# Kernel tuning notes

Hardware: AMD Instinct MI355X
Metric: run time of the kernel (lower is better)

The kernel has to match this reference:

```python
import jax, jax.numpy as jnp
import numpy as np

N = 38332          # poi_len - 1 nodes
POI_LEN = 38333
GF = 64            # graph_features
POI_DIM = 128
C = 128            # gcn_channel
L = 4              # gcn_layers
OUT = 128          # graph_out_dim
E = N * 16         # edges (avg degree 16)
IN_DIM = POI_DIM * GF // 2 + GF // 2  # 4128


def leaky(x, s):
    return jnp.where(x >= 0, x, s * x)


def _gcn(x, W, b, src, dst):
    # PyG GCNConv: lin -> symmetric deg^{-1/2} norm over self-loop graph -> scatter-sum + bias
    h = x @ W
    deg = jax.ops.segment_sum(jnp.ones(src.shape[0], h.dtype), dst, num_segments=N)
    dinv = jnp.where(deg > 0, jax.lax.rsqrt(deg), 0.0)
    norm = dinv[src] * dinv[dst]
    return jax.ops.segment_sum(h[src] * norm[:, None], dst, num_segments=N) + b


def _gat(x, W, a_src, a_dst, b, src, dst):
    # PyG GATConv (heads=1): per-edge LeakyReLU(0.2) logits, softmax over incoming edges
    h = x @ W
    als = h @ a_src            # [N]
    ald = h @ a_dst            # [N]
    e = leaky(als[src] + ald[dst], 0.2)   # [E+N]
    m = jax.ops.segment_max(e, dst, num_segments=N)
    ex = jnp.exp(e - m[dst])
    s = jax.ops.segment_sum(ex, dst, num_segments=N)
    alpha = ex / s[dst]
    return jax.ops.segment_sum(h[src] * alpha[:, None], dst, num_segments=N) + b


def _gnorm(x, w, b, ms, eps=1e-5):
    # PyG GraphNorm over the single graph (node axis)
    mean = x.mean(axis=0)
    out = x - ms * mean
    var = (out * out).mean(axis=0)
    return w * out * jax.lax.rsqrt(var + eps) + b


def setup_inputs() -> dict:
    key = jax.random.key(0)
    ks = jax.random.split(key, 20)
    d = {}
    d["poi"] = jax.random.randint(ks[0], (N, GF // 2), 0, POI_LEN, dtype=jnp.int32)
    d["distance"] = jax.random.uniform(ks[1], (N, GF // 2), dtype=jnp.float32)
    d["edge_index"] = jax.random.randint(ks[2], (2, E), 0, N, dtype=jnp.int32)
    d["emb_table"] = jax.random.normal(ks[3], (POI_LEN, POI_DIM), dtype=jnp.float32) * 0.05
    d["W_in"] = jax.random.normal(ks[4], (IN_DIM, C), dtype=jnp.float32) * 0.02
    d["b_in"] = jnp.zeros((C,), jnp.float32)
    d["gcn_W"] = jax.random.normal(ks[5], (L, C, C), dtype=jnp.float32) * 0.05
    d["gcn_b"] = jnp.zeros((L, C), jnp.float32)
    d["norm_w"] = jnp.ones((L, C), jnp.float32)
    d["norm_b"] = jnp.zeros((L, C), jnp.float32)
    d["norm_ms"] = jnp.ones((L, C), jnp.float32)
    d["gat_W"] = jax.random.normal(ks[6], (L, C, C), dtype=jnp.float32) * 0.05
    d["gat_asrc"] = jax.random.normal(ks[7], (L, C), dtype=jnp.float32) * 0.05
    d["gat_adst"] = jax.random.normal(ks[8], (L, C), dtype=jnp.float32) * 0.05
    d["gat_b"] = jnp.zeros((L, C), jnp.float32)
    d["W_out"] = jax.random.normal(ks[9], (C, 1), dtype=jnp.float32) * 0.05
    d["b_out"] = jnp.zeros((1,), jnp.float32)
    d["fc1_W"] = jax.random.normal(ks[10], (N, 128), dtype=jnp.float32) * 0.01
    d["fc1_b"] = jnp.zeros((128,), jnp.float32)
    d["fc2_W"] = jax.random.normal(ks[11], (128, OUT), dtype=jnp.float32) * 0.05
    d["fc2_b"] = jnp.zeros((OUT,), jnp.float32)
    return d


def reference(poi, distance, edge_index, emb_table, W_in, b_in, gcn_W, gcn_b,
              norm_w, norm_b, norm_ms, gat_W, gat_asrc, gat_adst, gat_b,
              W_out, b_out, fc1_W, fc1_b, fc2_W, fc2_b):
    loops = jnp.arange(N, dtype=edge_index.dtype)
    src = jnp.concatenate([edge_index[0], loops])   # self loops (PyG default)
    dst = jnp.concatenate([edge_index[1], loops])
    # feature assembly: emb(poi) flattened || distance
    x = jnp.concatenate([emb_table[poi].reshape(N, -1), distance], axis=1)  # [N, 4128]
    x = leaky(_gcn(x, W_in, b_in, src, dst), 0.01)
    for i in range(L):  # GcnUnit: GCN->norm->lrelu->res, GAT->norm->lrelu->res (shared norm params)
        t = _gnorm(_gcn(x, gcn_W[i], gcn_b[i], src, dst), norm_w[i], norm_b[i], norm_ms[i])
        x = x + leaky(t, 0.01)
        t = _gnorm(_gat(x, gat_W[i], gat_asrc[i], gat_adst[i], gat_b[i], src, dst),
                   norm_w[i], norm_b[i], norm_ms[i])
        x = x + leaky(t, 0.01)
    x = leaky(_gcn(x, W_out, b_out, src, dst), 0.01).reshape(-1)  # [N]
    h = leaky(x @ fc1_W + fc1_b, 0.01)
    return h @ fc2_W + fc2_b  # [128]
```

## Files before the change

kernel.cpp:

```cpp
#include <hip/hip_runtime.h>


typedef _Float16 f16;
typedef f16 f16x8 __attribute__((ext_vector_type(8)));
typedef f16 f16x4 __attribute__((ext_vector_type(4)));
typedef f16 f16x2 __attribute__((ext_vector_type(2)));
typedef float f32x4 __attribute__((ext_vector_type(4)));

__device__ __forceinline__ float lrelu(float x, float s){ return x>=0.f? x : s*x; }

__global__ __launch_bounds__(256) void k_deg(const int* __restrict__ dst,
                                             int* __restrict__ deg, int E) {
  int i = blockIdx.x * 256 + threadIdx.x;
  if (i < E) atomicAdd(&deg[dst[i]], 1);
}

__global__ __launch_bounds__(1024) void k_scan1(const int* __restrict__ deg,
    int* __restrict__ row_ptr, int* __restrict__ bsum, float* __restrict__ dinv, int n) {
  int b = blockIdx.x, t = threadIdx.x, i = b * 1024 + t;
  __shared__ int sd[1024];
  int v = (i < n) ? deg[i] : 0;
  if (i < n) dinv[i] = rsqrtf((float)(v + 1));
  sd[t] = v;
  __syncthreads();
  for (int off = 1; off < 1024; off <<= 1) {
    int o = (t >= off) ? sd[t - off] : 0;
    __syncthreads();
    sd[t] += o;
    __syncthreads();
  }
  if (i < n) row_ptr[i + 1] = sd[t];
  if (t == 1023) bsum[b] = sd[1023];
  if (b == 0 && t == 0) row_ptr[0] = 0;
}

__global__ __launch_bounds__(64) void k_scan2(int* __restrict__ bsum, int nb) {
  int lane = threadIdx.x;
  int v = (lane < nb) ? bsum[lane] : 0;
  int x = v;
  for (int off = 1; off < 64; off <<= 1) {
    int o = __shfl_up(x, off, 64);
    if (lane >= off) x += o;
  }
  if (lane < nb) bsum[lane] = x - v;
}

__global__ __launch_bounds__(256) void k_scan3(int* __restrict__ row_ptr,
                                               const int* __restrict__ bsum, int n) {
  int i = blockIdx.x * 256 + threadIdx.x;
  if (i < n) row_ptr[i + 1] += bsum[i >> 10];
}

__global__ __launch_bounds__(256) void k_fill(const int* __restrict__ src,
                                              const int* __restrict__ dst,
                                              const int* __restrict__ row_ptr,
                                              const float* __restrict__ dinv,
                                              int* __restrict__ fill,
                                              int* __restrict__ csr,
                                              float* __restrict__ csrw, int E) {
  int i = blockIdx.x * 256 + threadIdx.x;
  if (i < E) {
    int d = dst[i], s = src[i];
    int pos = row_ptr[d] + atomicAdd(&fill[d], 1);
    csr[pos] = s;
    csrw[pos] = dinv[d] * dinv[s];
  }
}

__global__ __launch_bounds__(256) void k_conv_emb(const float* __restrict__ src,
                                                  f16* __restrict__ dst, int total4) {
  int i = blockIdx.x * 256 + threadIdx.x;
  if (i >= total4) return;
  float4 v = ((const float4*)src)[i];
  f16x4 o = { (f16)v.x, (f16)v.y, (f16)v.z, (f16)v.w };
  ((f16x4*)dst)[i] = o;
}

__global__ __launch_bounds__(256) void k_pack_w(const float* __restrict__ W,
    f16* __restrict__ hi, int kb_total) {
  int idx = blockIdx.x * 256 + threadIdx.x;
  int c = idx & 127, kb = idx >> 7;
  if (kb >= kb_total) return;
  f16x8 hv;
#pragma unroll
  for (int j = 0; j < 8; j++) hv[j] = (f16)W[(size_t)(kb*8 + j) * 128 + c];
  ((f16x8*)hi)[idx] = hv;
}

__global__ __launch_bounds__(256) void k_pack_w8(const float* __restrict__ gcnW,
    const float* __restrict__ gatW, f16* __restrict__ hi, f16* __restrict__ lo) {
  int mat = blockIdx.y;
  const float* W = (mat < 4) ? gcnW + (size_t)mat * 16384 : gatW + (size_t)(mat - 4) * 16384;
  int idx = blockIdx.x * 256 + threadIdx.x;
  int c = idx & 127, kb = idx >> 7;
  f16x8 hv, lv;
#pragma unroll
  for (int j = 0; j < 8; j++) {
    float v = W[(size_t)(kb*8 + j) * 128 + c];
    f16 h = (f16)v;
    hv[j] = h; lv[j] = (f16)(v - (float)h);
  }
  ((f16x8*)hi)[mat * 2048 + idx] = hv;
  ((f16x8*)lo)[mat * 2048 + idx] = lv;
}

#define APAD 152
__global__ __launch_bounds__(512) void k_mfma_embed(const int* __restrict__ poi,
    const float* __restrict__ dist, const f16* __restrict__ eh,
    const f16* __restrict__ wh, f16* __restrict__ H16, int n) {
  __shared__ __attribute__((aligned(16))) char smem[49152];
  int* poi_s = (int*)smem;
  f16* aS    = (f16*)(smem + 8192);
  f16* OT    = (f16*)smem;
  float* F   = (float*)(smem + 16384);
  int tid = threadIdx.x;
  int bn = blockIdx.x * 64;
  int half = tid >> 8;
  int t2 = tid & 255;
  int ln = t2 >> 2, qt = t2 & 3;
  int xrow = bn + ln; if (xrow > n - 1) xrow = n - 1;
  {
#pragma unroll
    for (int jj = 0; jj < 4; jj++)
      poi_s[half * 1024 + (qt * 4 + jj) * 64 + ln] =
        poi[(size_t)xrow * 32 + half * 16 + qt * 4 + jj];
  }
  int w2 = (tid >> 6) & 3, lane = tid & 63;
  int q = lane >> 4, l15 = lane & 15;
  int mtb = (w2 & 1) * 2;
  int ntb = (w2 >> 1) * 4;
  f16* aH = aS + half * 64 * APAD;
  f32x4 acc[2][4];
#pragma unroll
  for (int a = 0; a < 2; a++)
#pragma unroll
    for (int b = 0; b < 4; b++) { acc[a][b][0]=0.f; acc[a][b][1]=0.f; acc[a][b][2]=0.f; acc[a][b][3]=0.f; }
  __syncthreads();

  f16x8 r0, r1, r2, r3;
  {
    const f16* srcp = eh + (size_t)poi_s[half * 1024 + ln] * 128 + qt * 32;
    r0 = *(const f16x8*)(srcp);      r1 = *(const f16x8*)(srcp + 8);
    r2 = *(const f16x8*)(srcp + 16); r3 = *(const f16x8*)(srcp + 24);
  }

#pragma unroll 1
  for (int j = 0; j < 16; j++) {
    __syncthreads();
    f16* wp = aH + ln * APAD + qt * 32;
    *(f16x8*)(wp) = r0; *(f16x8*)(wp + 8) = r1;
    *(f16x8*)(wp + 16) = r2; *(f16x8*)(wp + 24) = r3;
    if (j + 1 < 16) {
      const f16* srcp = eh + (size_t)poi_s[half * 1024 + (j + 1) * 64 + ln] * 128 + qt * 32;
      r0 = *(const f16x8*)(srcp);      r1 = *(const f16x8*)(srcp + 8);
      r2 = *(const f16x8*)(srcp + 16); r3 = *(const f16x8*)(srcp + 24);
    }
    __syncthreads();
#pragma unroll
    for (int kcl = 0; kcl < 4; kcl++) {
      f16x8 a_h[2];
#pragma unroll
      for (int mi = 0; mi < 2; mi++)
        a_h[mi] = *(const f16x8*)(aH + ((mtb + mi) * 16 + l15) * APAD + kcl * 32 + q * 8);
      int kb = (half * 16 + j) * 16 + kcl * 4 + q;
#pragma unroll
      for (int ni = 0; ni < 4; ni++) {
        f16x8 bh = *(const f16x8*)(wh + ((size_t)kb * 128 + (ntb + ni) * 16 + l15) * 8);
#pragma unroll
        for (int mi = 0; mi < 2; mi++)
          acc[mi][ni] = __builtin_amdgcn_mfma_f32_16x16x32_f16(a_h[mi], bh, acc[mi][ni], 0, 0, 0);
      }
    }
  }
  if (half) {
    int nc0 = bn + (mtb + 0) * 16 + l15; if (nc0 > n - 1) nc0 = n - 1;
    int nc1 = bn + (mtb + 1) * 16 + l15; if (nc1 > n - 1) nc1 = n - 1;
    f16x8 ad[2];
#pragma unroll
    for (int mi = 0; mi < 2; mi++) {
      int nc = mi ? nc1 : nc0;
      const float* dp = dist + (size_t)nc * 32 + q * 8;
      float4 d0 = *(const float4*)dp, d1 = *(const float4*)(dp + 4);
      ad[mi][0]=(f16)d0.x; ad[mi][1]=(f16)d0.y; ad[mi][2]=(f16)d0.z; ad[mi][3]=(f16)d0.w;
      ad[mi][4]=(f16)d1.x; ad[mi][5]=(f16)d1.y; ad[mi][6]=(f16)d1.z; ad[mi][7]=(f16)d1.w;
    }
    int kb = 512 + q;
#pragma unroll
    for (int ni = 0; ni < 4; ni++) {
      f16x8 bh = *(const f16x8*)(wh + ((size_t)kb * 128 + (ntb + ni) * 16 + l15) * 8);
#pragma unroll
      for (int mi = 0; mi < 2; mi++)
        acc[mi][ni] = __builtin_amdgcn_mfma_f32_16x16x32_f16(ad[mi], bh, acc[mi][ni], 0, 0, 0);
    }
  }
  __syncthreads();
  if (half) {
#pragma unroll
    for (int mi = 0; mi < 2; mi++)
#pragma unroll
      for (int ni = 0; ni < 4; ni++)
#pragma unroll
        for (int r = 0; r < 4; r++)
          F[((mtb + mi) * 16 + q * 4 + r) * 128 + (ntb + ni) * 16 + l15] = acc[mi][ni][r];
  }
  __syncthreads();
  if (!half) {
#pragma unroll
    for (int mi = 0; mi < 2; mi++)
#pragma unroll
      for (int ni = 0; ni < 4; ni++)
#pragma unroll
        for (int r = 0; r < 4; r++) {
          int o = ((mtb + mi) * 16 + q * 4 + r) * 128 + (ntb + ni) * 16 + l15;
          OT[o] = (f16)(acc[mi][ni][r] + F[o]);
        }
  }
  __syncthreads();
#pragma unroll
  for (int ch = 0; ch < 2; ch++) {
    int c1024 = tid + ch * 512;
    int row = c1024 >> 4, c8 = c1024 & 15;
    if (bn + row < n)
      *(f16x8*)(H16 + (size_t)(bn + row) * 128 + c8 * 8) = *(const f16x8*)(OT + row * 128 + c8 * 8);
  }
}

#define LPAD 136
__global__ __launch_bounds__(256) void k_mfma_lin(const f16* __restrict__ XH,
    const f16* __restrict__ wh, const f16* __restrict__ wl,
    f16* __restrict__ H16, int n,
    const float* __restrict__ asrc, const float* __restrict__ adst,
    float* __restrict__ als, float* __restrict__ ald) {
  __shared__ __attribute__((aligned(16))) char smem[64 * LPAD * 2];
  f16* aS = (f16*)smem;
  f16* ot = (f16*)smem;
  float* dsrc = (float*)(smem + 16384);
  float* ddst = (float*)(smem + 16896);
  int tid = threadIdx.x;
  int bn = blockIdx.x * 64;
  int ln = tid >> 2, qt = tid & 3;
  int xrow = bn + ln; if (xrow > n - 1) xrow = n - 1;
  int w = tid >> 6, lane = tid & 63;
  int q = lane >> 4, l15 = lane & 15;
  int mtb = (w & 1) * 2;
  int ntb = (w >> 1) * 4;
  {
    const f16* srcp = XH + (size_t)xrow * 128 + qt * 32;
    f16* wp = aS + ln * LPAD + qt * 32;
    *(f16x8*)(wp)      = *(const f16x8*)(srcp);
    *(f16x8*)(wp + 8)  = *(const f16x8*)(srcp + 8);
    *(f16x8*)(wp + 16) = *(const f16x8*)(srcp + 16);
    *(f16x8*)(wp + 24) = *(const f16x8*)(srcp + 24);
  }
  float av[4], bv[4];
  if (asrc) {
#pragma unroll
    for (int ni = 0; ni < 4; ni++) {
      av[ni] = asrc[(ntb + ni) * 16 + l15];
      bv[ni] = adst[(ntb + ni) * 16 + l15];
    }
  }
  f32x4 acc[2][4];
#pragma unroll
  for (int a = 0; a < 2; a++)
#pragma unroll
    for (int b = 0; b < 4; b++) { acc[a][b][0]=0.f; acc[a][b][1]=0.f; acc[a][b][2]=0.f; acc[a][b][3]=0.f; }
  __syncthreads();
#pragma unroll
  for (int kcl = 0; kcl < 4; kcl++) {
    f16x8 a_h[2];
#pragma unroll
    for (int mi = 0; mi < 2; mi++)
      a_h[mi] = *(const f16x8*)(aS + ((mtb + mi) * 16 + l15) * LPAD + kcl * 32 + q * 8);
    int kb = kcl * 4 + q;
#pragma unroll
    for (int ni = 0; ni < 4; ni++) {
      size_t boff = ((size_t)kb * 128 + (ntb + ni) * 16 + l15) * 8;
      f16x8 bh = *(const f16x8*)(wh + boff);
      f16x8 bl = *(const f16x8*)(wl + boff);
#pragma unroll
      for (int mi = 0; mi < 2; mi++) {
        acc[mi][ni] = __builtin_amdgcn_mfma_f32_16x16x32_f16(a_h[mi], bh, acc[mi][ni], 0, 0, 0);
        acc[mi][ni] = __builtin_amdgcn_mfma_f32_16x16x32_f16(a_h[mi], bl, acc[mi][ni], 0, 0, 0);
      }
    }
  }
  __syncthreads();
  if (asrc) {
#pragma unroll
    for (int mi = 0; mi < 2; mi++)
#pragma unroll
      for (int r = 0; r < 4; r++) {
        float ps = 0.f, pd = 0.f;
#pragma unroll
        for (int ni = 0; ni < 4; ni++) { ps += acc[mi][ni][r] * av[ni]; pd += acc[mi][ni][r] * bv[ni]; }
#pragma unroll
        for (int msk = 8; msk > 0; msk >>= 1) {
          ps += __shfl_xor(ps, msk, 64);
          pd += __shfl_xor(pd, msk, 64);
        }
        if (l15 == 0) {
          int row = (mtb + mi) * 16 + q * 4 + r;
          dsrc[row * 2 + (w >> 1)] = ps;
          ddst[row * 2 + (w >> 1)] = pd;
        }
      }
  }
#pragma unroll
  for (int mi = 0; mi < 2; mi++)
#pragma unroll
    for (int ni = 0; ni < 4; ni++)
#pragma unroll
      for (int r = 0; r < 4; r++)
        ot[((mtb + mi) * 16 + q * 4 + r) * 128 + (ntb + ni) * 16 + l15] = (f16)acc[mi][ni][r];
  __syncthreads();
  if (bn + ln < n) {
    f16* dst = H16 + (size_t)(bn + ln) * 128 + qt * 32;
    const f16* srcp = ot + ln * 128 + qt * 32;
#pragma unroll
    for (int jj = 0; jj < 4; jj++)
      *(f16x8*)(dst + jj * 8) = *(const f16x8*)(srcp + jj * 8);
  }
  if (asrc && tid < 64 && bn + tid < n) {
    als[bn + tid] = dsrc[tid * 2] + dsrc[tid * 2 + 1];
    ald[bn + tid] = ddst[tid * 2] + ddst[tid * 2 + 1];
  }
}

__global__ __launch_bounds__(256) void k_gcn_agg16(const f16x2* __restrict__ H2,
    const float* __restrict__ dinv, const int* __restrict__ row_ptr,
    const int* __restrict__ csr, const float* __restrict__ csrw,
    const float* __restrict__ bias,
    float2* __restrict__ out2, f16x2* __restrict__ xh_out, int n, int leaky_flag,
    float* __restrict__ psum, float* __restrict__ psumsq) {
  int w = threadIdx.x >> 6;
  int node = blockIdx.x * 4 + w;
  int lane = threadIdx.x & 63;
  __shared__ float s1[4][128], s2[4][128];
  float vx = 0.f, vy = 0.f;
  if (node < n) {
    int rs = row_ptr[node], re = row_ptr[node + 1];
    int d = re - rs;
    float dn = dinv[node];
    int  sidx = (lane < d) ? csr[rs + lane]  : 0;
    float swt = (lane < d) ? csrw[rs + lane] : 0.f;
    f16x2 sv = H2[(size_t)node * 64 + lane];
    float ax = dn * dn * (float)sv[0], ay = dn * dn * (float)sv[1];
    int dl = d < 64 ? d : 64;
    int j = 0;
#pragma unroll 4
    for (; j + 3 < dl; j += 4) {
      int i0 = __shfl(sidx, j, 64), i1 = __shfl(sidx, j + 1, 64);
      int i2 = __shfl(sidx, j + 2, 64), i3 = __shfl(sidx, j + 3, 64);
      float w0 = __shfl(swt, j, 64), w1 = __shfl(swt, j + 1, 64);
      float w2 = __shfl(swt, j + 2, 64), w3 = __shfl(swt, j + 3, 64);
      f16x2 v0 = H2[(size_t)i0 * 64 + lane];
      f16x2 v1 = H2[(size_t)i1 * 64 + lane];
      f16x2 v2 = H2[(size_t)i2 * 64 + lane];
      f16x2 v3 = H2[(size_t)i3 * 64 + lane];
      ax += w0*(float)v0[0] + w1*(float)v1[0] + w2*(float)v2[0] + w3*(float)v3[0];
      ay += w0*(float)v0[1] + w1*(float)v1[1] + w2*(float)v2[1] + w3*(float)v3[1];
    }
    for (; j < dl; j++) {
      int ii = __shfl(sidx, j, 64);
      float ww = __shfl(swt, j, 64);
      f16x2 v = H2[(size_t)ii * 64 + lane];
      ax += ww * (float)v[0]; ay += ww * (float)v[1];
    }
    for (int e = rs + 64; e < re; e++) {
      int s = csr[e]; float wv = csrw[e];
      f16x2 v = H2[(size_t)s * 64 + lane];
      ax += wv * (float)v[0]; ay += wv * (float)v[1];
    }
    float2 bvv = ((const float2*)bias)[lane];
    vx = ax + bvv.x; vy = ay + bvv.y;
    if (leaky_flag) { vx = lrelu(vx, 0.01f); vy = lrelu(vy, 0.01f); }
    out2[(size_t)node * 64 + lane] = make_float2(vx, vy);
    if (xh_out) { f16x2 o = { (f16)vx, (f16)vy }; xh_out[(size_t)node * 64 + lane] = o; }
  }
  if (psum) {
    s1[w][2*lane] = vx;  s1[w][2*lane+1] = vy;
    s2[w][2*lane] = vx*vx; s2[w][2*lane+1] = vy*vy;
    __syncthreads();
    int t = threadIdx.x;
    if (t < 128) {
      float S = s1[0][t] + s1[1][t] + s1[2][t] + s1[3][t];
      float Q = s2[0][t] + s2[1][t] + s2[2][t] + s2[3][t];
      int slot = blockIdx.x & 127;
      atomicAdd(&psum[slot * 128 + t], S);
      atomicAdd(&psumsq[slot * 128 + t], Q);
    }
  }
}

__global__ __launch_bounds__(256) void k_gat_agg16(const f16x2* __restrict__ H2,
    const float* __restrict__ als, const float* __restrict__ ald,
    const int* __restrict__ row_ptr, const int* __restrict__ csr,
    const float* __restrict__ bias, float2* __restrict__ y2, int n,
    float* __restrict__ psum, float* __restrict__ psumsq) {
  int w = threadIdx.x >> 6;
  int node = blockIdx.x * 4 + w;
  int lane = threadIdx.x & 63;
  __shared__ float s1[4][128], s2[4][128];
  float vx = 0.f, vy = 0.f;
  if (node < n) {
    int rs = row_ptr[node], re = row_ptr[node + 1];
    int d = re - rs;
    float aldn = ald[node];
    float e_self = lrelu(als[node] + aldn, 0.2f);
    f16x2 sv = H2[(size_t)node * 64 + lane];
    float ax, ay, sm;
    if (d <= 64) {
      int sidx = (lane < d) ? csr[rs + lane] : 0;
      float e_k = (lane < d) ? lrelu(als[sidx] + aldn, 0.2f) : -3.4e38f;
      float tmx = e_k;
      for (int off = 1; off < 64; off <<= 1) tmx = fmaxf(tmx, __shfl_xor(tmx, off, 64));
      float mx = fmaxf(e_self, tmx);
      float g_k = (lane < d) ? __expf(e_k - mx) : 0.f;
      float tsm = g_k;
      for (int off = 1; off < 64; off <<= 1) tsm += __shfl_xor(tsm, off, 64);
      float ws = __expf(e_self - mx);
      sm = tsm + ws;
      ax = ws * (float)sv[0]; ay = ws * (float)sv[1];
      int j = 0;
#pragma unroll 4
      for (; j + 3 < d; j += 4) {
        int i0 = __shfl(sidx, j, 64), i1 = __shfl(sidx, j + 1, 64);
        int i2 = __shfl(sidx, j + 2, 64), i3 = __shfl(sidx, j + 3, 64);
        float g0 = __shfl(g_k, j, 64), g1 = __shfl(g_k, j + 1, 64);
        float g2 = __shfl(g_k, j + 2, 64), g3 = __shfl(g_k, j + 3, 64);
        f16x2 v0 = H2[(size_t)i0 * 64 + lane];
        f16x2 v1 = H2[(size_t)i1 * 64 + lane];
        f16x2 v2 = H2[(size_t)i2 * 64 + lane];
        f16x2 v3 = H2[(size_t)i3 * 64 + lane];
        ax += g0*(float)v0[0] + g1*(float)v1[0] + g2*(float)v2[0] + g3*(float)v3[0];
        ay += g0*(float)v0[1] + g1*(float)v1[1] + g2*(float)v2[1] + g3*(float)v3[1];
      }
      for (; j < d; j++) {
        int ii = __shfl(sidx, j, 64);
        float gg = __shfl(g_k, j, 64);
        f16x2 v = H2[(size_t)ii * 64 + lane];
        ax += gg * (float)v[0]; ay += gg * (float)v[1];
      }
    } else {
      float mx = e_self;
      for (int i = rs + lane; i < re; i += 64) mx = fmaxf(mx, lrelu(als[csr[i]] + aldn, 0.2f));
      for (int off = 1; off < 64; off <<= 1) mx = fmaxf(mx, __shfl_xor(mx, off, 64));
      float ws = __expf(e_self - mx);
      sm = ws;
      ax = ws * (float)sv[0]; ay = ws * (float)sv[1];
      for (int i = rs; i < re; i++) {
        int s = csr[i];
        float g = __expf(lrelu(als[s] + aldn, 0.2f) - mx);
        f16x2 v = H2[(size_t)s * 64 + lane];
        sm += g; ax += g*(float)v[0]; ay += g*(float)v[1];
      }
    }
    float inv_s = 1.f / sm;
    float2 bvv = ((const float2*)bias)[lane];
    vx = ax * inv_s + bvv.x; vy = ay * inv_s + bvv.y;
    y2[(size_t)node * 64 + lane] = make_float2(vx, vy);
  }
  s1[w][2*lane] = vx;  s1[w][2*lane+1] = vy;
  s2[w][2*lane] = vx*vx; s2[w][2*lane+1] = vy*vy;
  __syncthreads();
  int t = threadIdx.x;
  if (t < 128) {
    float S = s1[0][t] + s1[1][t] + s1[2][t] + s1[3][t];
    float Q = s2[0][t] + s2[1][t] + s2[2][t] + s2[3][t];
    int slot = blockIdx.x & 127;
    atomicAdd(&psum[slot * 128 + t], S);
    atomicAdd(&psumsq[slot * 128 + t], Q);
  }
}

__global__ __launch_bounds__(256) void k_stats(const float* __restrict__ psum,
    const float* __restrict__ psumsq, const float* __restrict__ w,
    const float* __restrict__ bb, const float* __restrict__ ms,
    float* __restrict__ scaleA, float* __restrict__ shiftA, int n) {
  int t = threadIdx.x, c = t & 127, half = t >> 7;
  float S = 0.f, Q = 0.f;
  for (int s = half; s < 128; s += 2) { S += psum[s * 128 + c]; Q += psumsq[s * 128 + c]; }
  __shared__ float sh[256], sq[256];
  sh[t] = S; sq[t] = Q;
  __syncthreads();
  if (half == 0) {
    double Sd = (double)sh[c] + (double)sh[c + 128];
    double Qd = (double)sq[c] + (double)sq[c + 128];
    double invn = 1.0 / (double)n;
    double mean = Sd * invn;
    double mt = (double)ms[c] * mean;
    double var = Qd * invn - 2.0 * mt * mean + mt * mt;
    float rstd = rsqrtf((float)var + 1e-5f);
    float sc = w[c] * rstd;
    scaleA[c] = sc;
    shiftA[c] = bb[c] - sc * (float)mt;
  }
}

__global__ __launch_bounds__(256) void k_residual(const float* __restrict__ y,
    const float* __restrict__ scaleA, const float* __restrict__ shiftA,
    float* __restrict__ x, f16x4* __restrict__ xh, int n4) {
  int i = blockIdx.x * 256 + threadIdx.x;
  if (i >= n4) return;
  int c4 = (i & 31) * 4;
  float4 yv = ((const float4*)y)[i];
  float4 xv = ((float4*)x)[i];
  float4 sc = *(const float4*)(scaleA + c4);
  float4 sh = *(const float4*)(shiftA + c4);
  xv.x += lrelu(sc.x * yv.x + sh.x, 0.01f);
  xv.y += lrelu(sc.y * yv.y + sh.y, 0.01f);
  xv.z += lrelu(sc.z * yv.z + sh.z, 0.01f);
  xv.w += lrelu(sc.w * yv.w + sh.w, 0.01f);
  ((float4*)x)[i] = xv;
  if (xh) { f16x4 o = { (f16)xv.x, (f16)xv.y, (f16)xv.z, (f16)xv.w }; xh[i] = o; }
}

__global__ __launch_bounds__(256) void k_dot1(const float* __restrict__ x,
                                              const float* __restrict__ wv,
                                              float* __restrict__ o, int n) {
  int node = blockIdx.x * 4 + (threadIdx.x >> 6);
  int lane = threadIdx.x & 63;
  if (node >= n) return;
  float2 hv = ((const float2*)x)[(size_t)node * 64 + lane];
  float2 v1 = ((const float2*)wv)[lane];
  float s1 = hv.x * v1.x + hv.y * v1.y;
  for (int off = 32; off > 0; off >>= 1) s1 += __shfl_down(s1, off, 64);
  if (lane == 0) o[node] = s1;
}

__global__ __launch_bounds__(256) void k_scalar_agg(const float* __restrict__ xsv,
    const float* __restrict__ dinv, const int* __restrict__ row_ptr,
    const int* __restrict__ csr, const float* __restrict__ csrw,
    const float* __restrict__ b_out, float* __restrict__ xout, int n) {
  int i = blockIdx.x * 256 + threadIdx.x;
  if (i >= n) return;
  float dn = dinv[i];
  float acc = dn * dn * xsv[i];
  int re = row_ptr[i + 1];
  for (int e = row_ptr[i]; e < re; e++)
    acc += csrw[e] * xsv[csr[e]];
  xout[i] = lrelu(acc + b_out[0], 0.01f);
}

__global__ __launch_bounds__(256) void k_fc1(const float* __restrict__ xout,
    const float* __restrict__ fw, float* __restrict__ pfc, int n, int chunk) {
  int b = blockIdx.x, t = threadIdx.x;
  int c = t & 127, half = t >> 7;
  int s0 = b * chunk;
  int s1 = s0 + chunk; if (s1 > n) s1 = n;
  float s = 0.f;
  for (int i = s0 + half; i < s1; i += 2) s += xout[i] * fw[(size_t)i * 128 + c];
  __shared__ float sh[256];
  sh[t] = s; __syncthreads();
  if (half == 0) pfc[b * 128 + c] = sh[c] + sh[c + 128];
}

__global__ __launch_bounds__(128) void k_final(const float* __restrict__ pfc,
    const float* __restrict__ b1, const float* __restrict__ fw2,
    const float* __restrict__ b2, float* __restrict__ out) {
  int c = threadIdx.x;
  float s = 0.f;
  for (int b = 0; b < 128; b++) s += pfc[b * 128 + c];
  float hv = lrelu(s + b1[c], 0.01f);
  __shared__ float h1[128];
  h1[c] = hv; __syncthreads();
  float o = b2[c];
  for (int j = 0; j < 128; j++) o += h1[j] * fw2[j * 128 + c];
  out[c] = o;
}

extern "C" void kernel_launch(void* const* d_in, const int* in_sizes, int n_in,
                              void* d_out, int out_size, void* d_ws, size_t ws_size,
                              hipStream_t stream) {
  const int* poi      = (const int*)d_in[0];
  const float* dist   = (const float*)d_in[1];
  const int* ei       = (const int*)d_in[2];
  const float* emb    = (const float*)d_in[3];
  const float* W_in   = (const float*)d_in[4];
  const float* b_in   = (const float*)d_in[5];
  const float* gcn_W  = (const float*)d_in[6];
  const float* gcn_b  = (const float*)d_in[7];
  const float* norm_w = (const float*)d_in[8];
  const float* norm_b = (const float*)d_in[9];
  const float* norm_ms= (const float*)d_in[10];
  const float* gat_W  = (const float*)d_in[11];
  const float* gat_as = (const float*)d_in[12];
  const float* gat_ad = (const float*)d_in[13];
  const float* gat_b  = (const float*)d_in[14];
  const float* W_out  = (const float*)d_in[15];
  const float* b_out  = (const float*)d_in[16];
  const float* fc1_W  = (const float*)d_in[17];
  const float* fc1_b  = (const float*)d_in[18];
  const float* fc2_W  = (const float*)d_in[19];
  const float* fc2_b  = (const float*)d_in[20];

  const int N   = in_sizes[0] / 32;
  const int E   = in_sizes[2] / 2;
  const int POI = in_sizes[3] / 128;
  const int* srcp = ei;
  const int* dstp = ei + E;
  float* out = (float*)d_out;

  char* p = (char*)d_ws;
  auto alloc = [&](size_t bytes) { char* r = p; p += (bytes + 255) & ~(size_t)255; return r; };
  float* x   = (float*)alloc((size_t)N * 128 * 4);
  f16* h16   = (f16*)alloc((size_t)N * 128 * 2);
  f16* xh    = (f16*)alloc((size_t)N * 128 * 2);
  size_t Rneed = (size_t)POI * 128 * 2;
  size_t Ry    = (size_t)N * 128 * 4;
  char* R = alloc(Rneed > Ry ? Rneed : Ry);
  f16* ehalf = (f16*)R;
  float* y   = (float*)R;
  const int KBIN = 4128 / 8;
  f16* wih = (f16*)alloc((size_t)KBIN * 128 * 8 * 2);
  f16* wsh = (f16*)alloc((size_t)8 * 16384 * 2);
  f16* wsl = (f16*)alloc((size_t)8 * 16384 * 2);
  float* dinv   = (float*)alloc((size_t)N * 4);
  float* als    = (float*)alloc((size_t)N * 4);
  float* ald    = (float*)alloc((size_t)N * 4);
  float* xsv    = (float*)alloc((size_t)N * 4);
  float* xout   = (float*)alloc((size_t)N * 4);
  float* statsbuf = (float*)alloc((size_t)32 * 16384 * 4);
  float* pfc    = (float*)alloc(128 * 128 * 4);
  float* scaleA = (float*)alloc(128 * 4);
  float* shiftA = (float*)alloc(128 * 4);
  int* deg     = (int*)alloc((size_t)N * 2 * 4);
  int* fill    = deg + N;
  int* row_ptr = (int*)alloc(((size_t)N + 1) * 4);
  int* csr     = (int*)alloc((size_t)E * 4);
  float* csrw  = (float*)alloc((size_t)E * 4);
  int* bsum    = (int*)alloc(64 * 4);

  const int chunk = (N + 127) / 128;
  const int gblocks = (N + 63) / 64;
  const int eblocks = (E + 255) / 256;
  const int n4 = N * 32;
  const int nwb = (N + 3) / 4;
  const int nb1024 = (N + 1023) / 1024;

  hipMemsetAsync(deg, 0, sizeof(int) * 2 * (size_t)N, stream);
  hipMemsetAsync(statsbuf, 0, (size_t)32 * 16384 * 4, stream);
  k_deg<<<eblocks, 256, 0, stream>>>(dstp, deg, E);
  k_scan1<<<nb1024, 1024, 0, stream>>>(deg, row_ptr, bsum, dinv, N);
  k_scan2<<<1, 64, 0, stream>>>(bsum, nb1024);
  k_scan3<<<(N + 255) / 256, 256, 0, stream>>>(row_ptr, bsum, N);
  k_fill<<<eblocks, 256, 0, stream>>>(srcp, dstp, row_ptr, dinv, fill, csr, csrw, E);

  int et4 = POI * 128 / 4;
  k_conv_emb<<<(et4 + 255) / 256, 256, 0, stream>>>(emb, ehalf, et4);
  k_pack_w<<<(KBIN * 128 + 255) / 256, 256, 0, stream>>>(W_in, wih, KBIN);
  k_pack_w8<<<dim3(8, 8), 256, 0, stream>>>(gcn_W, gat_W, wsh, wsl);

  k_mfma_embed<<<gblocks, 512, 0, stream>>>(poi, dist, ehalf, wih, h16, N);
  k_gcn_agg16<<<nwb, 256, 0, stream>>>((const f16x2*)h16, dinv, row_ptr, csr, csrw, b_in,
                                       (float2*)x, (f16x2*)xh, N, 1, nullptr, nullptr);

  for (int l = 0; l < 4; l++) {
    const f16* gh = wsh + (size_t)l * 16384;
    const f16* gl = wsl + (size_t)l * 16384;
    const f16* th = wsh + (size_t)(4 + l) * 16384;
    const f16* tl = wsl + (size_t)(4 + l) * 16384;
    float* ps0 = statsbuf + (size_t)(4 * l) * 16384;
    float* pq0 = ps0 + 16384;
    float* ps1 = ps0 + 2 * 16384;
    float* pq1 = ps0 + 3 * 16384;
    k_mfma_lin<<<gblocks, 256, 0, stream>>>(xh, gh, gl, h16, N,
                                            (const float*)nullptr, (const float*)nullptr,
                                            (float*)nullptr, (float*)nullptr);
    k_gcn_agg16<<<nwb, 256, 0, stream>>>((const f16x2*)h16, dinv, row_ptr, csr, csrw,
                                         gcn_b + l * 128, (float2*)y, (f16x2*)nullptr, N, 0,
                                         ps0, pq0);
    k_stats<<<1, 256, 0, stream>>>(ps0, pq0, norm_w + l * 128, norm_b + l * 128,
                                   norm_ms + l * 128, scaleA, shiftA, N);
    k_residual<<<(n4 + 255) / 256, 256, 0, stream>>>(y, scaleA, shiftA, x, (f16x4*)xh, n4);
    k_mfma_lin<<<gblocks, 256, 0, stream>>>(xh, th, tl, h16, N,
                                            gat_as + l * 128, gat_ad + l * 128, als, ald);
    k_gat_agg16<<<nwb, 256, 0, stream>>>((const f16x2*)h16, als, ald, row_ptr, csr,
                                         gat_b + l * 128, (float2*)y, N, ps1, pq1);
    k_stats<<<1, 256, 0, stream>>>(ps1, pq1, norm_w + l * 128, norm_b + l * 128,
                                   norm_ms + l * 128, scaleA, shiftA, N);
    k_residual<<<(n4 + 255) / 256, 256, 0, stream>>>(y, scaleA, shiftA, x,
        (l == 3) ? (f16x4*)nullptr : (f16x4*)xh, n4);
  }

  k_dot1<<<nwb, 256, 0, stream>>>(x, W_out, xsv, N);
  k_scalar_agg<<<(N + 255) / 256, 256, 0, stream>>>(xsv, dinv, row_ptr, csr, csrw, b_out, xout, N);
  k_fc1<<<128, 256, 0, stream>>>(xout, fc1_W, pfc, N, chunk);
  k_final<<<1, 128, 0, stream>>>(pfc, fc1_b, fc2_W, fc2_b, out);
}
```

Measured before the change: 1.010 ms.

## Fuse residual/norm into linear loads, store aggregates as f16, widen gather

Removes the separate residual kernel: the GraphNorm scale/shift, leaky ReLU and residual add are now applied while the MFMA linear kernel loads its input tile, and for the last layer inside the final dot kernel. Aggregation outputs are stored as half precision instead of float32, and the f16 copy of x is dropped. The gather loops now have each half-wave process alternate edges with 4-wide f16 loads, combining the halves through a cross-lane shuffle. This cuts launches and intermediate memory traffic, at the cost of extra rounding from storing the normalized input in half precision.

Result: no change. 1.019 ms (+0.9%).

```diff
diff --git a/kernel.cpp b/kernel.cpp
--- a/kernel.cpp
+++ b/kernel.cpp
@@ -226,7 +226,9 @@
 }
 
 #define LPAD 136
-__global__ __launch_bounds__(256) void k_mfma_lin(const f16* __restrict__ XH,
+__global__ __launch_bounds__(256) void k_mfma_lin(float* __restrict__ X,
+    const f16* __restrict__ Y, const float* __restrict__ scaleA,
+    const float* __restrict__ shiftA,
     const f16* __restrict__ wh, const f16* __restrict__ wl,
     f16* __restrict__ H16, int n,
     const float* __restrict__ asrc, const float* __restrict__ adst,
@@ -239,18 +241,38 @@
   int tid = threadIdx.x;
   int bn = blockIdx.x * 64;
   int ln = tid >> 2, qt = tid & 3;
-  int xrow = bn + ln; if (xrow > n - 1) xrow = n - 1;
+  int xrow = bn + ln; bool valid = xrow < n; if (!valid) xrow = n - 1;
   int w = tid >> 6, lane = tid & 63;
   int q = lane >> 4, l15 = lane & 15;
   int mtb = (w & 1) * 2;
   int ntb = (w >> 1) * 4;
   {
-    const f16* srcp = XH + (size_t)xrow * 128 + qt * 32;
+    float* xp = X + (size_t)xrow * 128 + qt * 32;
     f16* wp = aS + ln * LPAD + qt * 32;
-    *(f16x8*)(wp)      = *(const f16x8*)(srcp);
-    *(f16x8*)(wp + 8)  = *(const f16x8*)(srcp + 8);
-    *(f16x8*)(wp + 16) = *(const f16x8*)(srcp + 16);
-    *(f16x8*)(wp + 24) = *(const f16x8*)(srcp + 24);
+    if (Y) {
+      const f16* yp = Y + (size_t)xrow * 128 + qt * 32;
+#pragma unroll
+      for (int cc = 0; cc < 32; cc += 4) {
+        float4 xv = *(const float4*)(xp + cc);
+        f16x4 yv = *(const f16x4*)(yp + cc);
+        float4 sc = *(const float4*)(scaleA + qt * 32 + cc);
+        float4 sh = *(const float4*)(shiftA + qt * 32 + cc);
+        xv.x += lrelu(sc.x * (float)yv[0] + sh.x, 0.01f);
+        xv.y += lrelu(sc.y * (float)yv[1] + sh.y, 0.01f);
+        xv.z += lrelu(sc.z * (float)yv[2] + sh.z, 0.01f);
+        xv.w += lrelu(sc.w * (float)yv[3] + sh.w, 0.01f);
+        if (valid) *(float4*)(xp + cc) = xv;
+        f16x4 st = { (f16)xv.x, (f16)xv.y, (f16)xv.z, (f16)xv.w };
+        *(f16x4*)(wp + cc) = st;
+      }
+    } else {
+#pragma unroll
+      for (int cc = 0; cc < 32; cc += 4) {
+        float4 xv = *(const float4*)(xp + cc);
+        f16x4 st = { (f16)xv.x, (f16)xv.y, (f16)xv.z, (f16)xv.w };
+        *(f16x4*)(wp + cc) = st;
+      }
+    }
   }
   float av[4], bv[4];
   if (asrc) {
@@ -327,60 +349,78 @@
   }
 }
 
-__global__ __launch_bounds__(256) void k_gcn_agg16(const f16x2* __restrict__ H2,
+__global__ __launch_bounds__(256) void k_gcn_agg16(const f16x4* __restrict__ H4,
     const float* __restrict__ dinv, const int* __restrict__ row_ptr,
     const int* __restrict__ csr, const float* __restrict__ csrw,
     const float* __restrict__ bias,
-    float2* __restrict__ out2, f16x2* __restrict__ xh_out, int n, int leaky_flag,
+    float4* __restrict__ xout4, f16x4* __restrict__ y4, int n, int leaky_flag,
     float* __restrict__ psum, float* __restrict__ psumsq) {
   int w = threadIdx.x >> 6;
   int node = blockIdx.x * 4 + w;
   int lane = threadIdx.x & 63;
+  int half = lane >> 5, li = lane & 31;
   __shared__ float s1[4][128], s2[4][128];
-  float vx = 0.f, vy = 0.f;
+  float o0=0.f,o1=0.f,o2=0.f,o3=0.f;
   if (node < n) {
     int rs = row_ptr[node], re = row_ptr[node + 1];
     int d = re - rs;
     float dn = dinv[node];
     int  sidx = (lane < d) ? csr[rs + lane]  : 0;
     float swt = (lane < d) ? csrw[rs + lane] : 0.f;
-    f16x2 sv = H2[(size_t)node * 64 + lane];
-    float ax = dn * dn * (float)sv[0], ay = dn * dn * (float)sv[1];
+    float a0, a1, a2, a3;
+    {
+      f16x4 v = H4[(size_t)node * 32 + li];
+      float wv = 0.5f * dn * dn;
+      a0 = wv*(float)v[0]; a1 = wv*(float)v[1]; a2 = wv*(float)v[2]; a3 = wv*(float)v[3];
+    }
     int dl = d < 64 ? d : 64;
     int j = 0;
-#pragma unroll 4
-    for (; j + 3 < dl; j += 4) {
-      int i0 = __shfl(sidx, j, 64), i1 = __shfl(sidx, j + 1, 64);
-      int i2 = __shfl(sidx, j + 2, 64), i3 = __shfl(sidx, j + 3, 64);
-      float w0 = __shfl(swt, j, 64), w1 = __shfl(swt, j + 1, 64);
-      float w2 = __shfl(swt, j + 2, 64), w3 = __shfl(swt, j + 3, 64);
-      f16x2 v0 = H2[(size_t)i0 * 64 + lane];
-      f16x2 v1 = H2[(size_t)i1 * 64 + lane];
-      f16x2 v2 = H2[(size_t)i2 * 64 + lane];
-      f16x2 v3 = H2[(size_t)i3 * 64 + lane];
-      ax += w0*(float)v0[0] + w1*(float)v1[0] + w2*(float)v2[0] + w3*(float)v3[0];
-      ay += w0*(float)v0[1] + w1*(float)v1[1] + w2*(float)v2[1] + w3*(float)v3[1];
-    }
-    for (; j < dl; j++) {
+    for (; j + 7 < dl; j += 8) {
+      int i0 = __shfl(sidx, j + half, 64),     i1 = __shfl(sidx, j + 2 + half, 64);
+      int i2 = __shfl(sidx, j + 4 + half, 64), i3 = __shfl(sidx, j + 6 + half, 64);
+      float w0 = __shfl(swt, j + half, 64),     w1 = __shfl(swt, j + 2 + half, 64);
+      float w2 = __shfl(swt, j + 4 + half, 64), w3 = __shfl(swt, j + 6 + half, 64);
+      f16x4 v0 = H4[(size_t)i0 * 32 + li];
+      f16x4 v1 = H4[(size_t)i1 * 32 + li];
+      f16x4 v2 = H4[(size_t)i2 * 32 + li];
+      f16x4 v3 = H4[(size_t)i3 * 32 + li];
+      a0 += w0*(float)v0[0] + w1*(float)v1[0] + w2*(float)v2[0] + w3*(float)v3[0];
+      a1 += w0*(float)v0[1] + w1*(float)v1[1] + w2*(float)v2[1] + w3*(float)v3[1];
+      a2 += w0*(float)v0[2] + w1*(float)v1[2] + w2*(float)v2[2] + w3*(float)v3[2];
+      a3 += w0*(float)v0[3] + w1*(float)v1[3] + w2*(float)v2[3] + w3*(float)v3[3];
+    }
+    for (; j + 1 < dl; j += 2) {
+      int ii = __shfl(sidx, j + half, 64);
+      float ww = __shfl(swt, j + half, 64);
+      f16x4 v = H4[(size_t)ii * 32 + li];
+      a0 += ww*(float)v[0]; a1 += ww*(float)v[1]; a2 += ww*(float)v[2]; a3 += ww*(float)v[3];
+    }
+    if (j < dl) {
       int ii = __shfl(sidx, j, 64);
-      float ww = __shfl(swt, j, 64);
-      f16x2 v = H2[(size_t)ii * 64 + lane];
-      ax += ww * (float)v[0]; ay += ww * (float)v[1];
+      float ww = 0.5f * __shfl(swt, j, 64);
+      f16x4 v = H4[(size_t)ii * 32 + li];
+      a0 += ww*(float)v[0]; a1 += ww*(float)v[1]; a2 += ww*(float)v[2]; a3 += ww*(float)v[3];
     }
     for (int e = rs + 64; e < re; e++) {
-      int s = csr[e]; float wv = csrw[e];
-      f16x2 v = H2[(size_t)s * 64 + lane];
-      ax += wv * (float)v[0]; ay += wv * (float)v[1];
-    }
-    float2 bvv = ((const float2*)bias)[lane];
-    vx = ax + bvv.x; vy = ay + bvv.y;
-    if (leaky_flag) { vx = lrelu(vx, 0.01f); vy = lrelu(vy, 0.01f); }
-    out2[(size_t)node * 64 + lane] = make_float2(vx, vy);
-    if (xh_out) { f16x2 o = { (f16)vx, (f16)vy }; xh_out[(size_t)node * 64 + lane] = o; }
+      int s = csr[e]; float wv = 0.5f * csrw[e];
+      f16x4 v = H4[(size_t)s * 32 + li];
+      a0 += wv*(float)v[0]; a1 += wv*(float)v[1]; a2 += wv*(float)v[2]; a3 += wv*(float)v[3];
+    }
+    a0 += __shfl_xor(a0, 32, 64); a1 += __shfl_xor(a1, 32, 64);
+    a2 += __shfl_xor(a2, 32, 64); a3 += __shfl_xor(a3, 32, 64);
+    if (half == 0) {
+      float4 bv = ((const float4*)bias)[li];
+      o0 = a0 + bv.x; o1 = a1 + bv.y; o2 = a2 + bv.z; o3 = a3 + bv.w;
+      if (leaky_flag) { o0 = lrelu(o0,0.01f); o1 = lrelu(o1,0.01f); o2 = lrelu(o2,0.01f); o3 = lrelu(o3,0.01f); }
+      if (xout4) xout4[(size_t)node * 32 + li] = make_float4(o0, o1, o2, o3);
+      if (y4) { f16x4 o = { (f16)o0, (f16)o1, (f16)o2, (f16)o3 }; y4[(size_t)node * 32 + li] = o; }
+    }
   }
   if (psum) {
-    s1[w][2*lane] = vx;  s1[w][2*lane+1] = vy;
-    s2[w][2*lane] = vx*vx; s2[w][2*lane+1] = vy*vy;
+    if (half == 0) {
+      s1[w][4*li+0]=o0; s1[w][4*li+1]=o1; s1[w][4*li+2]=o2; s1[w][4*li+3]=o3;
+      s2[w][4*li+0]=o0*o0; s2[w][4*li+1]=o1*o1; s2[w][4*li+2]=o2*o2; s2[w][4*li+3]=o3*o3;
+    }
     __syncthreads();
     int t = threadIdx.x;
     if (t < 128) {
@@ -393,23 +433,23 @@
   }
 }
 
-__global__ __launch_bounds__(256) void k_gat_agg16(const f16x2* __restrict__ H2,
+__global__ __launch_bounds__(256) void k_gat_agg16(const f16x4* __restrict__ H4,
     const float* __restrict__ als, const float* __restrict__ ald,
     const int* __restrict__ row_ptr, const int* __restrict__ csr,
-    const float* __restrict__ bias, float2* __restrict__ y2, int n,
+    const float* __restrict__ bias, f16x4* __restrict__ y4, int n,
     float* __restrict__ psum, float* __restrict__ psumsq) {
   int w = threadIdx.x >> 6;
   int node = blockIdx.x * 4 + w;
   int lane = threadIdx.x & 63;
+  int half = lane >> 5, li = lane & 31;
   __shared__ float s1[4][128], s2[4][128];
-  float vx = 0.f, vy = 0.f;
+  float o0=0.f,o1=0.f,o2=0.f,o3=0.f;
   if (node < n) {
     int rs = row_ptr[node], re = row_ptr[node + 1];
     int d = re - rs;
     float aldn = ald[node];
     float e_self = lrelu(als[node] + aldn, 0.2f);
-    f16x2 sv = H2[(size_t)node * 64 + lane];
-    float ax, ay, sm;
+    float a0, a1, a2, a3, sm;
     if (d <= 64) {
       int sidx = (lane < d) ? csr[rs + lane] : 0;
       float e_k = (lane < d) ? lrelu(als[sidx] + aldn, 0.2f) : -3.4e38f;
@@ -421,26 +461,37 @@
       for (int off = 1; off < 64; off <<= 1) tsm += __shfl_xor(tsm, off, 64);
       float ws = __expf(e_self - mx);
       sm = tsm + ws;
-      ax = ws * (float)sv[0]; ay = ws * (float)sv[1];
+      {
+        f16x4 v = H4[(size_t)node * 32 + li];
+        float wv = 0.5f * ws;
+        a0 = wv*(float)v[0]; a1 = wv*(float)v[1]; a2 = wv*(float)v[2]; a3 = wv*(float)v[3];
+      }
       int j = 0;
-#pragma unroll 4
-      for (; j + 3 < d; j += 4) {
-        int i0 = __shfl(sidx, j, 64), i1 = __shfl(sidx, j + 1, 64);
-        int i2 = __shfl(sidx, j + 2, 64), i3 = __shfl(sidx, j + 3, 64);
-        float g0 = __shfl(g_k, j, 64), g1 = __shfl(g_k, j + 1, 64);
-        float g2 = __shfl(g_k, j + 2, 64), g3 = __shfl(g_k, j + 3, 64);
-        f16x2 v0 = H2[(size_t)i0 * 64 + lane];
-        f16x2 v1 = H2[(size_t)i1 * 64 + lane];
-        f16x2 v2 = H2[(size_t)i2 * 64 + lane];
-        f16x2 v3 = H2[(size_t)i3 * 64 + lane];
-        ax += g0*(float)v0[0] + g1*(float)v1[0] + g2*(float)v2[0] + g3*(float)v3[0];
-        ay += g0*(float)v0[1] + g1*(float)v1[1] + g2*(float)v2[1] + g3*(float)v3[1];
-      }
-      for (; j < d; j++) {
+      for (; j + 7 < d; j += 8) {
+        int i0 = __shfl(sidx, j + half, 64),     i1 = __shfl(sidx, j + 2 + half, 64);
+        int i2 = __shfl(sidx, j + 4 + half, 64), i3 = __shfl(sidx, j + 6 + half, 64);
+        float g0 = __shfl(g_k, j + half, 64),     g1 = __shfl(g_k, j + 2 + half, 64);
+        float g2 = __shfl(g_k, j + 4 + half, 64), g3 = __shfl(g_k, j + 6 + half, 64);
+        f16x4 v0 = H4[(size_t)i0 * 32 + li];
+        f16x4 v1 = H4[(size_t)i1 * 32 + li];
+        f16x4 v2 = H4[(size_t)i2 * 32 + li];
+        f16x4 v3 = H4[(size_t)i3 * 32 + li];
+        a0 += g0*(float)v0[0] + g1*(float)v1[0] + g2*(float)v2[0] + g3*(float)v3[0];
+        a1 += g0*(float)v0[1] + g1*(float)v1[1] + g2*(float)v2[1] + g3*(float)v3[1];
+        a2 += g0*(float)v0[2] + g1*(float)v1[2] + g2*(float)v2[2] + g3*(float)v3[2];
+        a3 += g0*(float)v0[3] + g1*(float)v1[3] + g2*(float)v2[3] + g3*(float)v3[3];
+      }
+      for (; j + 1 < d; j += 2) {
+        int ii = __shfl(sidx, j + half, 64);
+        float gg = __shfl(g_k, j + half, 64);
+        f16x4 v = H4[(size_t)ii * 32 + li];
+        a0 += gg*(float)v[0]; a1 += gg*(float)v[1]; a2 += gg*(float)v[2]; a3 += gg*(float)v[3];
+      }
+      if (j < d) {
         int ii = __shfl(sidx, j, 64);
-        float gg = __shfl(g_k, j, 64);
-        f16x2 v = H2[(size_t)ii * 64 + lane];
-        ax += gg * (float)v[0]; ay += gg * (float)v[1];
+        float gg = 0.5f * __shfl(g_k, j, 64);
+        f16x4 v = H4[(size_t)ii * 32 + li];
+        a0 += gg*(float)v[0]; a1 += gg*(float)v[1]; a2 += gg*(float)v[2]; a3 += gg*(float)v[3];
       }
     } else {
       float mx = e_self;
@@ -448,21 +499,35 @@
       for (int off = 1; off < 64; off <<= 1) mx = fmaxf(mx, __shfl_xor(mx, off, 64));
       float ws = __expf(e_self - mx);
       sm = ws;
-      ax = ws * (float)sv[0]; ay = ws * (float)sv[1];
-      for (int i = rs; i < re; i++) {
-        int s = csr[i];
+      {
+        f16x4 v = H4[(size_t)node * 32 + li];
+        float wv = 0.5f * ws;
+        a0 = wv*(float)v[0]; a1 = wv*(float)v[1]; a2 = wv*(float)v[2]; a3 = wv*(float)v[3];
+      }
+      for (int e = rs; e < re; e++) {
+        int s = csr[e];
         float g = __expf(lrelu(als[s] + aldn, 0.2f) - mx);
-        f16x2 v = H2[(size_t)s * 64 + lane];
-        sm += g; ax += g*(float)v[0]; ay += g*(float)v[1];
-      }
-    }
-    float inv_s = 1.f / sm;
-    float2 bvv = ((const float2*)bias)[lane];
-    vx = ax * inv_s + bvv.x; vy = ay * inv_s + bvv.y;
-    y2[(size_t)node * 64 + lane] = make_float2(vx, vy);
-  }
-  s1[w][2*lane] = vx;  s1[w][2*lane+1] = vy;
-  s2[w][2*lane] = vx*vx; s2[w][2*lane+1] = vy*vy;
+        sm += g;
+        float gg = 0.5f * g;
+        f16x4 v = H4[(size_t)s * 32 + li];
+        a0 += gg*(float)v[0]; a1 += gg*(float)v[1]; a2 += gg*(float)v[2]; a3 += gg*(float)v[3];
+      }
+    }
+    a0 += __shfl_xor(a0, 32, 64); a1 += __shfl_xor(a1, 32, 64);
+    a2 += __shfl_xor(a2, 32, 64); a3 += __shfl_xor(a3, 32, 64);
+    if (half == 0) {
+      float inv_s = 1.f / sm;
+      float4 bv = ((const float4*)bias)[li];
+      o0 = a0 * inv_s + bv.x; o1 = a1 * inv_s + bv.y;
+      o2 = a2 * inv_s + bv.z; o3 = a3 * inv_s + bv.w;
+      f16x4 o = { (f16)o0, (f16)o1, (f16)o2, (f16)o3 };
+      y4[(size_t)node * 32 + li] = o;
+    }
+  }
+  if (half == 0) {
+    s1[w][4*li+0]=o0; s1[w][4*li+1]=o1; s1[w][4*li+2]=o2; s1[w][4*li+3]=o3;
+    s2[w][4*li+0]=o0*o0; s2[w][4*li+1]=o1*o1; s2[w][4*li+2]=o2*o2; s2[w][4*li+3]=o3*o3;
+  }
   __syncthreads();
   int t = threadIdx.x;
   if (t < 128) {
@@ -498,33 +563,21 @@
   }
 }
 
-__global__ __launch_bounds__(256) void k_residual(const float* __restrict__ y,
-    const float* __restrict__ scaleA, const float* __restrict__ shiftA,
-    float* __restrict__ x, f16x4* __restrict__ xh, int n4) {
-  int i = blockIdx.x * 256 + threadIdx.x;
-  if (i >= n4) return;
-  int c4 = (i & 31) * 4;
-  float4 yv = ((const float4*)y)[i];
-  float4 xv = ((float4*)x)[i];
-  float4 sc = *(const float4*)(scaleA + c4);
-  float4 sh = *(const float4*)(shiftA + c4);
-  xv.x += lrelu(sc.x * yv.x + sh.x, 0.01f);
-  xv.y += lrelu(sc.y * yv.y + sh.y, 0.01f);
-  xv.z += lrelu(sc.z * yv.z + sh.z, 0.01f);
-  xv.w += lrelu(sc.w * yv.w + sh.w, 0.01f);
-  ((float4*)x)[i] = xv;
-  if (xh) { f16x4 o = { (f16)xv.x, (f16)xv.y, (f16)xv.z, (f16)xv.w }; xh[i] = o; }
-}
-
-__global__ __launch_bounds__(256) void k_dot1(const float* __restrict__ x,
-                                              const float* __restrict__ wv,
-                                              float* __restrict__ o, int n) {
+__global__ __launch_bounds__(256) void k_dot1(const float2* __restrict__ x2,
+    const f16x2* __restrict__ y2, const float* __restrict__ scaleA,
+    const float* __restrict__ shiftA, const float* __restrict__ wv,
+    float* __restrict__ o, int n) {
   int node = blockIdx.x * 4 + (threadIdx.x >> 6);
   int lane = threadIdx.x & 63;
   if (node >= n) return;
-  float2 hv = ((const float2*)x)[(size_t)node * 64 + lane];
+  float2 xv = x2[(size_t)node * 64 + lane];
+  f16x2 yv = y2[(size_t)node * 64 + lane];
+  float2 sc = ((const float2*)scaleA)[lane];
+  float2 sh = ((const float2*)shiftA)[lane];
+  float a = xv.x + lrelu(sc.x * (float)yv[0] + sh.x, 0.01f);
+  float b = xv.y + lrelu(sc.y * (float)yv[1] + sh.y, 0.01f);
   float2 v1 = ((const float2*)wv)[lane];
-  float s1 = hv.x * v1.x + hv.y * v1.y;
+  float s1 = a * v1.x + b * v1.y;
   for (int off = 32; off > 0; off >>= 1) s1 += __shfl_down(s1, off, 64);
   if (lane == 0) o[node] = s1;
 }
@@ -606,12 +659,11 @@
   auto alloc = [&](size_t bytes) { char* r = p; p += (bytes + 255) & ~(size_t)255; return r; };
   float* x   = (float*)alloc((size_t)N * 128 * 4);
   f16* h16   = (f16*)alloc((size_t)N * 128 * 2);
-  f16* xh    = (f16*)alloc((size_t)N * 128 * 2);
   size_t Rneed = (size_t)POI * 128 * 2;
-  size_t Ry    = (size_t)N * 128 * 4;
+  size_t Ry    = (size_t)N * 128 * 2;
   char* R = alloc(Rneed > Ry ? Rneed : Ry);
   f16* ehalf = (f16*)R;
-  float* y   = (float*)R;
+  f16* y16   = (f16*)R;
   const int KBIN = 4128 / 8;
   f16* wih = (f16*)alloc((size_t)KBIN * 128 * 8 * 2);
   f16* wsh = (f16*)alloc((size_t)8 * 16384 * 2);
@@ -635,7 +687,6 @@
   const int chunk = (N + 127) / 128;
   const int gblocks = (N + 63) / 64;
   const int eblocks = (E + 255) / 256;
-  const int n4 = N * 32;
   const int nwb = (N + 3) / 4;
   const int nb1024 = (N + 1023) / 1024;
 
@@ -653,8 +704,8 @@
   k_pack_w8<<<dim3(8, 8), 256, 0, stream>>>(gcn_W, gat_W, wsh, wsl);
 
   k_mfma_embed<<<gblocks, 512, 0, stream>>>(poi, dist, ehalf, wih, h16, N);
-  k_gcn_agg16<<<nwb, 256, 0, stream>>>((const f16x2*)h16, dinv, row_ptr, csr, csrw, b_in,
-                                       (float2*)x, (f16x2*)xh, N, 1, nullptr, nullptr);
+  k_gcn_agg16<<<nwb, 256, 0, stream>>>((const f16x4*)h16, dinv, row_ptr, csr, csrw, b_in,
+                                       (float4*)x, (f16x4*)nullptr, N, 1, nullptr, nullptr);
 
   for (int l = 0; l < 4; l++) {
     const f16* gh = wsh + (size_t)l * 16384;
@@ -665,26 +716,25 @@
     float* pq0 = ps0 + 16384;
     float* ps1 = ps0 + 2 * 16384;
     float* pq1 = ps0 + 3 * 16384;
-    k_mfma_lin<<<gblocks, 256, 0, stream>>>(xh, gh, gl, h16, N,
+    k_mfma_lin<<<gblocks, 256, 0, stream>>>(x, (l == 0) ? (const f16*)nullptr : y16,
+                                            scaleA, shiftA, gh, gl, h16, N,
                                             (const float*)nullptr, (const float*)nullptr,
                                             (float*)nullptr, (float*)nullptr);
-    k_gcn_agg16<<<nwb, 256, 0, stream>>>((const f16x2*)h16, dinv, row_ptr, csr, csrw,
-                                         gcn_b + l * 128, (float2*)y, (f16x2*)nullptr, N, 0,
-                                         ps0, pq0);
+    k_gcn_agg16<<<nwb, 256, 0, stream>>>((const f16x4*)h16, dinv, row_ptr, csr, csrw,
+                                         gcn_b + l * 128, (float4*)nullptr, (f16x4*)y16,
+                                         N, 0, ps0, pq0);
     k_stats<<<1, 256, 0, stream>>>(ps0, pq0, norm_w + l * 128, norm_b + l * 128,
                                    norm_ms + l * 128, scaleA, shiftA, N);
-    k_residual<<<(n4 + 255) / 256, 256, 0, stream>>>(y, scaleA, shiftA, x, (f16x4*)xh, n4);
-    k_mfma_lin<<<gblocks, 256, 0, stream>>>(xh, th, tl, h16, N,
+    k_mfma_lin<<<gblocks, 256, 0, stream>>>(x, y16, scaleA, shiftA, th, tl, h16, N,
                                             gat_as + l * 128, gat_ad + l * 128, als, ald);
-    k_gat_agg16<<<nwb, 256, 0, stream>>>((const f16x2*)h16, als, ald, row_ptr, csr,
-                                         gat_b + l * 128, (float2*)y, N, ps1, pq1);
+    k_gat_agg16<<<nwb, 256, 0, stream>>>((const f16x4*)h16, als, ald, row_ptr, csr,
+                                         gat_b + l * 128, (f16x4*)y16, N, ps1, pq1);
     k_stats<<<1, 256, 0, stream>>>(ps1, pq1, norm_w + l * 128, norm_b + l * 128,
                                    norm_ms + l * 128, scaleA, shiftA, N);
-    k_residual<<<(n4 + 255) / 256, 256, 0, stream>>>(y, scaleA, shiftA, x,
-        (l == 3) ? (f16x4*)nullptr : (f16x4*)xh, n4);
-  }
-
-  k_dot1<<<nwb, 256, 0, stream>>>(x, W_out, xsv, N);
+  }
+
+  k_dot1<<<nwb, 256, 0, stream>>>((const float2*)x, (const f16x2*)y16, scaleA, shiftA,
+                                  W_out, xsv, N);
   k_scalar_agg<<<(N + 255) / 256, 256, 0, stream>>>(xsv, dinv, row_ptr, csr, csrw, b_out, xout, N);
   k_fc1<<<128, 256, 0, stream>>>(xout, fc1_W, pfc, N, chunk);
   k_final<<<1, 128, 0, stream>>>(pfc, fc1_b, fc2_W, fc2_b, out);
```
